# Kernel tuning notes

Hardware: AMD Instinct MI355X
Metric: run time of the kernel (lower is better)

Reference implementation:

```python
import jax, jax.numpy as jnp
import numpy as np

D_MODEL = 1024
N_HEADS = 16
D_K = D_MODEL // N_HEADS
SIGMA = 1.0
NUM_ITERS = 3
PAD_POS = 10000.0


def setup_inputs() -> dict:
    rng = jax.random.key(0)
    ks = jax.random.split(rng, 16)
    B, Lq, Lk = 8, 512, 512
    s = 1.0 / np.sqrt(D_MODEL).astype(np.float32)
    return {
        "query": jax.random.normal(ks[0], (B, Lq, D_MODEL), jnp.float32),
        "key": jax.random.normal(ks[1], (B, Lk, D_MODEL), jnp.float32),
        "value": jax.random.normal(ks[2], (B, Lk, D_MODEL), jnp.float32),
        "query_lengths": jax.random.randint(ks[3], (B,), 2, Lq),
        "key_lengths": jax.random.randint(ks[4], (B,), 2, Lk),
        "Wq": jax.random.normal(ks[5], (D_MODEL, D_MODEL), jnp.float32) * s,
        "bq": jnp.zeros((D_MODEL,), jnp.float32),
        "Wk": jax.random.normal(ks[6], (D_MODEL, D_MODEL), jnp.float32) * s,
        "bk": jnp.zeros((D_MODEL,), jnp.float32),
        "Wv": jax.random.normal(ks[7], (D_MODEL, D_MODEL), jnp.float32) * s,
        "bv": jnp.zeros((D_MODEL,), jnp.float32),
        "Wo": jax.random.normal(ks[8], (D_MODEL, D_MODEL), jnp.float32) * s,
        "bo": jnp.zeros((D_MODEL,), jnp.float32),
        "pos_scale": jnp.ones((1,), jnp.float32),
        "pos_bias": jnp.zeros((1,), jnp.float32),
    }


def _init_positions(lengths, max_len, scale, bias):
    # vectorized tcr_pep init: linspace(-L/2, L/2, L) per row, pad -> 10000
    j = jnp.arange(max_len, dtype=jnp.float32)[None, :]          # [1, L]
    L = lengths.astype(jnp.float32)[:, None]                      # [B, 1]
    step = jnp.where(L > 1.0, L / (L - 1.0), 0.0)                 # linspace step
    pos = (-L / 2.0 + j * step) * scale + bias
    pad = jnp.arange(max_len)[None, :] >= lengths[:, None]
    return jnp.where(pad, PAD_POS, pos)


def _distance_attention(qp, kp):
    d2 = (qp[:, :, None] - kp[:, None, :]) ** 2                   # [B, Lq, Lk]
    attn = jnp.exp(-d2 / (2.0 * SIGMA * SIGMA))
    masked = (qp[:, :, None] >= 1000.0) | (kp[:, None, :] >= 1000.0)
    return jnp.where(masked, 0.0, attn)


def _update_positions(qp, kp, attn):
    qn = attn / jnp.clip(attn.sum(-1, keepdims=True), 1e-9)
    qp_new = jnp.einsum('bqk,bk->bq', qn, kp)
    at = attn.transpose(0, 2, 1)
    kn = at / jnp.clip(at.sum(-1, keepdims=True), 1e-9)
    kp_new = jnp.einsum('bkq,bq->bk', kn, qp)
    qp_new = jnp.where(qp >= 1000.0, PAD_POS, qp_new)
    kp_new = jnp.where(kp >= 1000.0, PAD_POS, kp_new)
    return qp_new, kp_new


def reference(query, key, value, query_lengths, key_lengths,
              Wq, bq, Wk, bk, Wv, bv, Wo, bo, pos_scale, pos_bias):
    B, Lq, _ = query.shape
    Lk = key.shape[1]

    def split_heads(x):
        return x.reshape(B, -1, N_HEADS, D_K).transpose(0, 2, 1, 3)  # [B,H,L,Dk]

    q = split_heads(query @ Wq.T + bq)
    k = split_heads(key @ Wk.T + bk)
    v = split_heads(value @ Wv.T + bv)

    qp = _init_positions(query_lengths, Lq, pos_scale, pos_bias)  # [B, Lq]
    kp = _init_positions(key_lengths, Lk, pos_scale, pos_bias)    # [B, Lk]

    scores = jnp.einsum('bhqd,bhkd->bhqk', q, k) / jnp.sqrt(jnp.float32(D_K))
    attn = jax.nn.softmax(scores, axis=-1)                        # [B,H,Lq,Lk]

    for _ in range(NUM_ITERS):
        da = _distance_attention(qp, kp)                          # [B,Lq,Lk]
        comb = attn * da[:, None, :, :]
        comb = comb / jnp.clip(comb.sum(-1, keepdims=True), 1e-9)
        qp, kp = _update_positions(qp, kp, da)
        attn = comb

    ctx = jnp.einsum('bhqk,bhkd->bhqd', attn, v)
    ctx = ctx.transpose(0, 2, 1, 3).reshape(B, Lq, D_MODEL)
    out = ctx @ Wo.T + bo
    return out, attn.mean(axis=1)
```

## Files before the change

### kernel.cpp

```cpp
#include <hip/hip_runtime.h>
#include <math.h>

#define B_  8
#define LQ  512
#define LK  512
#define DM  1024
#define NH  16
#define DK  64
constexpr float PADP = 10000.0f;

typedef short s16x8 __attribute__((ext_vector_type(8)));
typedef float f32x4 __attribute__((ext_vector_type(4)));

__device__ inline unsigned short f2b1(float f) {
    unsigned u = __float_as_uint(f);
    unsigned r = (u + 0x7fffu + ((u >> 16) & 1u)) >> 16;
    return (unsigned short)r;
}

__global__ __launch_bounds__(256) void f2b_kernel(
    const float* __restrict__ in, unsigned short* __restrict__ out, int n4)
{
    const int i = blockIdx.x * 256 + threadIdx.x;
    if (i >= n4) return;
    const float4 v = *(const float4*)&in[(size_t)i * 4];
    ushort4 o;
    o.x = f2b1(v.x); o.y = f2b1(v.y); o.z = f2b1(v.z); o.w = f2b1(v.w);
    *(ushort4*)&out[(size_t)i * 4] = o;
}

__global__ __launch_bounds__(512) void posInit_kernel(
    const int* __restrict__ qlen, const int* __restrict__ klen,
    const float* __restrict__ pscale, const float* __restrict__ pbias,
    float* __restrict__ posQ, float* __restrict__ posK)
{
    const int b = blockIdx.x, t = threadIdx.x;
    const float scale = pscale[0], bias = pbias[0];
    {
        int ql = qlen[b];
        float Lf = (float)ql;
        float step = (Lf > 1.0f) ? Lf / (Lf - 1.0f) : 0.0f;
        float pos = (-Lf * 0.5f + (float)t * step) * scale + bias;
        posQ[b * LQ + t] = (t >= ql) ? PADP : pos;
    }
    {
        int kl = klen[b];
        float Lf = (float)kl;
        float step = (Lf > 1.0f) ? Lf / (Lf - 1.0f) : 0.0f;
        float pos = (-Lf * 0.5f + (float)t * step) * scale + bias;
        posK[b * LK + t] = (t >= kl) ? PADP : pos;
    }
}

template <bool SUMS>
__global__ __launch_bounds__(512) void daRow_kernel(
    const float* __restrict__ posQ, const float* __restrict__ posK,
    float* __restrict__ Db,
    float* __restrict__ rsB, float* __restrict__ rdB,
    float* __restrict__ colS, float* __restrict__ colD)
{
    constexpr int NCH = 16, QC = LQ / NCH;
    __shared__ float kpl[LK];
    __shared__ float csp[8][LK], cdp[8][LK];
    const int chunk = blockIdx.x, b = blockIdx.y;
    const int t = threadIdx.x, w = t >> 6, lane = t & 63;
    kpl[t] = posK[b * LK + t];
    __syncthreads();

    float cs[8] = {0,0,0,0,0,0,0,0}, cd[8] = {0,0,0,0,0,0,0,0};
    float* Dbb = Db + (size_t)b * LQ * LK;

    for (int qi = chunk * QC + w; qi < chunk * QC + QC; qi += 8) {
        const float qpv = posQ[b * LQ + qi];
        const bool qpad = (qpv >= 1000.0f);
        float rsum = 0.0f, rdot = 0.0f;
#pragma unroll
        for (int c = 0; c < 8; ++c) {
            const int k = lane + 64 * c;
            const float kpv = kpl[k];
            const float d = qpv - kpv;
            float e = (qpad || (kpv >= 1000.0f)) ? 0.0f : __expf(-0.5f * d * d);
            if (SUMS) { rsum += e; rdot += e * kpv; cs[c] += e; cd[c] += e * qpv; }
            Dbb[(size_t)qi * LK + k] = e;
        }
        if (SUMS) {
#pragma unroll
            for (int o = 32; o > 0; o >>= 1) {
                rsum += __shfl_xor(rsum, o);
                rdot += __shfl_xor(rdot, o);
            }
            if (lane == 0) { rsB[b * LQ + qi] = rsum; rdB[b * LQ + qi] = rdot; }
        }
    }
    if (SUMS) {
#pragma unroll
        for (int c = 0; c < 8; ++c) {
            csp[w][lane + 64 * c] = cs[c];
            cdp[w][lane + 64 * c] = cd[c];
        }
        __syncthreads();
        float s = 0.0f, dd = 0.0f;
        for (int ww = 0; ww < 8; ++ww) { s += csp[ww][t]; dd += cdp[ww][t]; }
        colS[((size_t)b * NCH + chunk) * LK + t] = s;
        colD[((size_t)b * NCH + chunk) * LK + t] = dd;
    }
}

__global__ __launch_bounds__(512) void posUpd_kernel(
    float* __restrict__ posQ, float* __restrict__ posK,
    const float* __restrict__ rsB, const float* __restrict__ rdB,
    const float* __restrict__ colS, const float* __restrict__ colD)
{
    constexpr int NCH = 16;
    const int b = blockIdx.x, t = threadIdx.x;
    float colsum = 0.0f, coldot = 0.0f;
#pragma unroll
    for (int c = 0; c < NCH; ++c) {
        colsum += colS[((size_t)b * NCH + c) * LK + t];
        coldot += colD[((size_t)b * NCH + c) * LK + t];
    }
    const float nk = (posK[b * LK + t] >= 1000.0f) ? PADP : coldot / fmaxf(colsum, 1e-9f);
    const float nq = (posQ[b * LQ + t] >= 1000.0f) ? PADP : rdB[b * LQ + t] / fmaxf(rsB[b * LQ + t], 1e-9f);
    posQ[b * LQ + t] = nq;
    posK[b * LK + t] = nk;
}

__global__ __launch_bounds__(256) void transpose_bf16(
    const unsigned short* __restrict__ in, unsigned short* __restrict__ out,
    int Mn, int Nn)
{
    __shared__ unsigned short tile[64][65];
    const int m0 = blockIdx.y * 64, n0 = blockIdx.x * 64;
    const int t = threadIdx.x;
    const int r = t >> 3, c8 = (t & 7) * 8;
#pragma unroll
    for (int rr = 0; rr < 64; rr += 32) {
        const uint4 v = *(const uint4*)&in[(size_t)(m0 + r + rr) * Nn + n0 + c8];
        const unsigned short* pv = (const unsigned short*)&v;
#pragma unroll
        for (int j = 0; j < 8; ++j) tile[r + rr][c8 + j] = pv[j];
    }
    __syncthreads();
#pragma unroll
    for (int rr = 0; rr < 64; rr += 32) {
        unsigned short tmp[8];
#pragma unroll
        for (int j = 0; j < 8; ++j) tmp[j] = tile[c8 + j][r + rr];
        *(uint4*)&out[(size_t)(n0 + r + rr) * Mn + m0 + c8] = *(uint4*)tmp;
    }
}

template <bool OB>
__global__ __launch_bounds__(256) void gemm_bf16_nt(
    const unsigned short* __restrict__ A,
    const unsigned short* __restrict__ Bt,
    void* __restrict__ Cv,
    const float* __restrict__ bias,
    int M, int N, int K, float alpha)
{
    constexpr int BKP = 40;
    __shared__ short As[64 * BKP];
    __shared__ short Bs[128 * BKP];
    const int m0 = blockIdx.y * 64, n0 = blockIdx.x * 128;
    const int t = threadIdx.x;
    const int wid = t >> 6, lane = t & 63;
    const int wr = wid >> 1, wc = wid & 1;
    const int lr = lane & 15, lk = (lane >> 4) * 8;

    f32x4 acc[2][4] = {};

    const int arow = t >> 2, aseg = (t & 3) * 8;
    const int brow = t >> 1, bseg = (t & 1) * 16;

    for (int kb = 0; kb < K; kb += 32) {
        const uint4 av  = *(const uint4*)&A[(size_t)(m0 + arow) * K + kb + aseg];
        const uint4 bv0 = *(const uint4*)&Bt[(size_t)(n0 + brow) * K + kb + bseg];
        const uint4 bv1 = *(const uint4*)&Bt[(size_t)(n0 + brow) * K + kb + bseg + 8];
        __syncthreads();
        *(uint4*)&As[arow * BKP + aseg] = av;
        *(uint4*)&Bs[brow * BKP + bseg] = bv0;
        *(uint4*)&Bs[brow * BKP + bseg + 8] = bv1;
        __syncthreads();

        s16x8 af[2], bf[4];
#pragma unroll
        for (int i = 0; i < 2; ++i)
            af[i] = *(const s16x8*)&As[(wr * 32 + i * 16 + lr) * BKP + lk];
#pragma unroll
        for (int j = 0; j < 4; ++j)
            bf[j] = *(const s16x8*)&Bs[(wc * 64 + j * 16 + lr) * BKP + lk];
#pragma unroll
        for (int i = 0; i < 2; ++i)
#pragma unroll
            for (int j = 0; j < 4; ++j)
                acc[i][j] = __builtin_amdgcn_mfma_f32_16x16x32_bf16(
                    af[i], bf[j], acc[i][j], 0, 0, 0);
    }

    const int r0 = (lane >> 4) * 4;
#pragma unroll
    for (int i = 0; i < 2; ++i) {
        const int row = m0 + wr * 32 + i * 16 + r0;
#pragma unroll
        for (int j = 0; j < 4; ++j) {
            const int col = n0 + wc * 64 + j * 16 + lr;
            const float bvv = bias ? bias[col] : 0.0f;
#pragma unroll
            for (int r = 0; r < 4; ++r) {
                const float val = acc[i][j][r] * alpha + bvv;
                if (OB) ((unsigned short*)Cv)[(size_t)(row + r) * N + col] = f2b1(val);
                else    ((float*)Cv)[(size_t)(row + r) * N + col] = val;
            }
        }
    }
}

__global__ __launch_bounds__(256) void scores_mfma(
    const unsigned short* __restrict__ Qb,
    const unsigned short* __restrict__ Kb,
    float* __restrict__ S, int hbase)
{
    constexpr int BKP = 72;
    __shared__ short As[128 * BKP];
    __shared__ short Bs[128 * BKP];
    const int z = blockIdx.z;
    const int b = z >> 3, hh = z & 7;
    const int hcol = (hbase + hh) * DK;
    const int m0 = blockIdx.y * 128, n0 = blockIdx.x * 128;
    const int t = threadIdx.x;
    const int wid = t >> 6, lane = t & 63;
    const int wr = wid >> 1, wc = wid & 1;
    const int lr = lane & 15, lk = (lane >> 4) * 8;

    const int srow = t >> 1, sseg = (t & 1) * 32;
    {
        const unsigned short* ag = &Qb[((size_t)(b * LQ + m0 + srow)) * DM + hcol + sseg];
        const unsigned short* bg = &Kb[((size_t)(b * LK + n0 + srow)) * DM + hcol + sseg];
#pragma unroll
        for (int s = 0; s < 4; ++s) {
            *(uint4*)&As[srow * BKP + sseg + s * 8] = *(const uint4*)(ag + s * 8);
            *(uint4*)&Bs[srow * BKP + sseg + s * 8] = *(const uint4*)(bg + s * 8);
        }
    }
    __syncthreads();

    f32x4 acc[4][4] = {};
#pragma unroll
    for (int kh = 0; kh < 2; ++kh) {
        s16x8 af[4], bf[4];
#pragma unroll
        for (int i = 0; i < 4; ++i)
            af[i] = *(const s16x8*)&As[(wr * 64 + i * 16 + lr) * BKP + kh * 32 + lk];
#pragma unroll
        for (int j = 0; j < 4; ++j)
            bf[j] = *(const s16x8*)&Bs[(wc * 64 + j * 16 + lr) * BKP + kh * 32 + lk];
#pragma unroll
        for (int i = 0; i < 4; ++i)
#pragma unroll
            for (int j = 0; j < 4; ++j)
                acc[i][j] = __builtin_amdgcn_mfma_f32_16x16x32_bf16(
                    af[i], bf[j], acc[i][j], 0, 0, 0);
    }

    const int r0 = (lane >> 4) * 4;
#pragma unroll
    for (int i = 0; i < 4; ++i) {
        const int row = m0 + wr * 64 + i * 16 + r0;
#pragma unroll
        for (int j = 0; j < 4; ++j) {
            const int col = n0 + wc * 64 + j * 16 + lr;
#pragma unroll
            for (int r = 0; r < 4; ++r)
                S[((size_t)z * LQ + row + r) * LK + col] = acc[i][j][r] * 0.125f;
        }
    }
}

__global__ __launch_bounds__(256) void ctx_mfma(
    const unsigned short* __restrict__ Ab,
    const unsigned short* __restrict__ VbT,
    unsigned short* __restrict__ ctxb, int hbase)
{
    constexpr int BKP = 72;
    __shared__ short As[64 * BKP];
    __shared__ short Bs[64 * BKP];
    const int z = blockIdx.z;
    const int b = z >> 3, hh = z & 7;
    const int hcol = (hbase + hh) * DK;
    const int q0 = blockIdx.y * 64;
    const int t = threadIdx.x;
    const int wid = t >> 6, lane = t & 63;
    const int wr = wid >> 1, wc = wid & 1;
    const int lr = lane & 15, lk = (lane >> 4) * 8;

    const unsigned short* Abase = Ab + ((size_t)z * LQ + q0) * LK;
    const unsigned short* Bbase = VbT + (size_t)hcol * (B_ * LK) + (size_t)b * LK;

    f32x4 acc[2][2] = {};
    const int srow = t >> 2, sseg = (t & 3) * 16;

    for (int kb = 0; kb < LK; kb += 64) {
        const uint4 a0 = *(const uint4*)&Abase[(size_t)srow * LK + kb + sseg];
        const uint4 a1 = *(const uint4*)&Abase[(size_t)srow * LK + kb + sseg + 8];
        const uint4 b0 = *(const uint4*)&Bbase[(size_t)srow * (B_ * LK) + kb + sseg];
        const uint4 b1 = *(const uint4*)&Bbase[(size_t)srow * (B_ * LK) + kb + sseg + 8];
        __syncthreads();
        *(uint4*)&As[srow * BKP + sseg] = a0;
        *(uint4*)&As[srow * BKP + sseg + 8] = a1;
        *(uint4*)&Bs[srow * BKP + sseg] = b0;
        *(uint4*)&Bs[srow * BKP + sseg + 8] = b1;
        __syncthreads();

#pragma unroll
        for (int kh = 0; kh < 2; ++kh) {
            s16x8 af[2], bf[2];
#pragma unroll
            for (int i = 0; i < 2; ++i)
                af[i] = *(const s16x8*)&As[(wr * 32 + i * 16 + lr) * BKP + kh * 32 + lk];
#pragma unroll
            for (int j = 0; j < 2; ++j)
                bf[j] = *(const s16x8*)&Bs[(wc * 32 + j * 16 + lr) * BKP + kh * 32 + lk];
#pragma unroll
            for (int i = 0; i < 2; ++i)
#pragma unroll
                for (int j = 0; j < 2; ++j)
                    acc[i][j] = __builtin_amdgcn_mfma_f32_16x16x32_bf16(
                        af[i], bf[j], acc[i][j], 0, 0, 0);
        }
    }

    const int r0 = (lane >> 4) * 4;
#pragma unroll
    for (int i = 0; i < 2; ++i) {
        const int row = b * LQ + q0 + wr * 32 + i * 16 + r0;
#pragma unroll
        for (int j = 0; j < 2; ++j) {
            const int col = hcol + wc * 32 + j * 16 + lr;
#pragma unroll
            for (int r = 0; r < 4; ++r)
                ctxb[(size_t)(row + r) * DM + col] = f2b1(acc[i][j][r]);
        }
    }
}

template <bool BT>
__global__ __launch_bounds__(256) void gemm64(
    const float* __restrict__ A, int lda, long aS1, long aS2,
    const float* __restrict__ Bm, int ldb, long bS1, long bS2,
    float* __restrict__ C, int ldc, long cS1, long cS2,
    const float* __restrict__ bias, int K, float alpha, int zshift)
{
    const int z = blockIdx.z;
    const long z1 = z >> zshift;
    const long z2 = z & ((1 << zshift) - 1);
    A  += z1 * aS1 + z2 * aS2;
    Bm += z1 * bS1 + z2 * bS2;
    C  += z1 * cS1 + z2 * cS2;

    const int m0 = blockIdx.y * 64, n0 = blockIdx.x * 64;
    __shared__ float As[32][68];
    __shared__ float Bs[32][68];
    const int t = threadIdx.x;
    const int ty = t >> 4, tx = t & 15;

    float acc[4][4];
#pragma unroll
    for (int i = 0; i < 4; ++i)
#pragma unroll
        for (int j = 0; j < 4; ++j) acc[i][j] = 0.0f;

    const int mA = t >> 3;
    const int kA = (t & 7) * 4;

    for (int kb = 0; kb < K; kb += 32) {
        {
            const float4 a0 = *(const float4*)&A[(size_t)(m0 + mA) * lda + kb + kA];
            const float4 a1 = *(const float4*)&A[(size_t)(m0 + mA + 32) * lda + kb + kA];
            As[kA + 0][mA] = a0.x; As[kA + 1][mA] = a0.y; As[kA + 2][mA] = a0.z; As[kA + 3][mA] = a0.w;
            As[kA + 0][mA + 32] = a1.x; As[kA + 1][mA + 32] = a1.y; As[kA + 2][mA + 32] = a1.z; As[kA + 3][mA + 32] = a1.w;
        }
        if (BT) {
            const float4 b0 = *(const float4*)&Bm[(size_t)(n0 + mA) * ldb + kb + kA];
            const float4 b1 = *(const float4*)&Bm[(size_t)(n0 + mA + 32) * ldb + kb + kA];
            Bs[kA + 0][mA] = b0.x; Bs[kA + 1][mA] = b0.y; Bs[kA + 2][mA] = b0.z; Bs[kA + 3][mA] = b0.w;
            Bs[kA + 0][mA + 32] = b1.x; Bs[kA + 1][mA + 32] = b1.y; Bs[kA + 2][mA + 32] = b1.z; Bs[kA + 3][mA + 32] = b1.w;
        } else {
            const int kB = t >> 4;
            const int nB = (t & 15) * 4;
            const float4 b0 = *(const float4*)&Bm[(size_t)(kb + kB) * ldb + n0 + nB];
            const float4 b1 = *(const float4*)&Bm[(size_t)(kb + kB + 16) * ldb + n0 + nB];
            *(float4*)&Bs[kB][nB] = b0;
            *(float4*)&Bs[kB + 16][nB] = b1;
        }
        __syncthreads();

#pragma unroll
        for (int kk = 0; kk < 32; ++kk) {
            const float4 av = *(const float4*)&As[kk][ty * 4];
            const float4 bv = *(const float4*)&Bs[kk][tx * 4];
            const float a[4] = {av.x, av.y, av.z, av.w};
            const float bb[4] = {bv.x, bv.y, bv.z, bv.w};
#pragma unroll
            for (int i = 0; i < 4; ++i)
#pragma unroll
                for (int j = 0; j < 4; ++j)
                    acc[i][j] = fmaf(a[i], bb[j], acc[i][j]);
        }
        __syncthreads();
    }

#pragma unroll
    for (int i = 0; i < 4; ++i) {
        const int row = m0 + ty * 4 + i;
        float4 o;
        o.x = acc[i][0] * alpha;
        o.y = acc[i][1] * alpha;
        o.z = acc[i][2] * alpha;
        o.w = acc[i][3] * alpha;
        if (bias) {
            o.x += bias[n0 + tx * 4 + 0];
            o.y += bias[n0 + tx * 4 + 1];
            o.z += bias[n0 + tx * 4 + 2];
            o.w += bias[n0 + tx * 4 + 3];
        }
        *(float4*)&C[(size_t)row * ldc + n0 + tx * 4] = o;
    }
}

template <bool BF16OUT>
__global__ __launch_bounds__(256) void softmaxP_kernel(
    float* __restrict__ S, const float* __restrict__ D,
    void* __restrict__ AOut, float* __restrict__ meanOut,
    int nheads, int accumulate)
{
    const int b = blockIdx.x >> 9, q = blockIdx.x & 511;
    const int t = threadIdx.x, w = t >> 6, lane = t & 63;
    __shared__ float Pl[3][LK];
    __shared__ float part[4][LK];
    const size_t NPB = (size_t)B_ * LQ * LK;
    const size_t rowoff = ((size_t)b * LQ + q) * LK;

    for (int i = t; i < LK; i += 256) {
        Pl[0][i] = D[rowoff + i];
        Pl[1][i] = D[NPB + rowoff + i];
        Pl[2][i] = D[2 * NPB + rowoff + i];
    }
    __syncthreads();

    float macc[8];
#pragma unroll
    for (int j = 0; j < 8; ++j) macc[j] = 0.0f;

    for (int h = w; h < nheads; h += 4) {
        const size_t roff = (((size_t)b * nheads + h) * LQ + q) * LK;
        const float* row = S + roff;
        float v[8];
        const float4 s0 = *(const float4*)&row[lane * 8];
        const float4 s1 = *(const float4*)&row[lane * 8 + 4];
        v[0] = s0.x; v[1] = s0.y; v[2] = s0.z; v[3] = s0.w;
        v[4] = s1.x; v[5] = s1.y; v[6] = s1.z; v[7] = s1.w;
        float mx = v[0];
#pragma unroll
        for (int j = 1; j < 8; ++j) mx = fmaxf(mx, v[j]);
#pragma unroll
        for (int o = 32; o > 0; o >>= 1) mx = fmaxf(mx, __shfl_xor(mx, o));
        float zz = 0.0f;
#pragma unroll
        for (int j = 0; j < 8; ++j) { v[j] = __expf(v[j] - mx); zz += v[j]; }
#pragma unroll
        for (int o = 32; o > 0; o >>= 1) zz += __shfl_xor(zz, o);
        const float invz = 1.0f / zz;
#pragma unroll
        for (int j = 0; j < 8; ++j) v[j] *= invz;

#pragma unroll
        for (int it = 0; it < 3; ++it) {
            float s = 0.0f;
#pragma unroll
            for (int j = 0; j < 8; ++j) {
                v[j] *= Pl[it][lane * 8 + j];
                s += v[j];
            }
#pragma unroll
            for (int o = 32; o > 0; o >>= 1) s += __shfl_xor(s, o);
            const float inv = 1.0f / fmaxf(s, 1e-9f);
#pragma unroll
            for (int j = 0; j < 8; ++j) v[j] *= inv;
        }

#pragma unroll
        for (int j = 0; j < 8; ++j) macc[j] += v[j];

        if (BF16OUT) {
            unsigned short* arow = (unsigned short*)AOut + roff;
            ushort4 u0, u1;
            u0.x = f2b1(v[0]); u0.y = f2b1(v[1]); u0.z = f2b1(v[2]); u0.w = f2b1(v[3]);
            u1.x = f2b1(v[4]); u1.y = f2b1(v[5]); u1.z = f2b1(v[6]); u1.w = f2b1(v[7]);
            *(ushort4*)&arow[lane * 8] = u0;
            *(ushort4*)&arow[lane * 8 + 4] = u1;
        } else {
            float* arow = (float*)AOut + roff;
            *(float4*)&arow[lane * 8] = make_float4(v[0], v[1], v[2], v[3]);
            *(float4*)&arow[lane * 8 + 4] = make_float4(v[4], v[5], v[6], v[7]);
        }
    }

    *(float4*)&part[w][lane * 8] = make_float4(macc[0], macc[1], macc[2], macc[3]);
    *(float4*)&part[w][lane * 8 + 4] = make_float4(macc[4], macc[5], macc[6], macc[7]);
    __syncthreads();

    for (int i = t; i < LK; i += 256) {
        const float m = (part[0][i] + part[1][i] + part[2][i] + part[3][i]) * (1.0f / 16.0f);
        const size_t oi = ((size_t)b * LQ + q) * LK + i;
        meanOut[oi] = accumulate ? (meanOut[oi] + m) : m;
    }
}

extern "C" void kernel_launch(void* const* d_in, const int* in_sizes, int n_in,
                              void* d_out, int out_size, void* d_ws, size_t ws_size,
                              hipStream_t stream)
{
    const float* query  = (const float*)d_in[0];
    const float* key    = (const float*)d_in[1];
    const float* value  = (const float*)d_in[2];
    const int*   qlen   = (const int*)d_in[3];
    const int*   klen   = (const int*)d_in[4];
    const float* Wq     = (const float*)d_in[5];
    const float* bq     = (const float*)d_in[6];
    const float* Wk     = (const float*)d_in[7];
    const float* bk     = (const float*)d_in[8];
    const float* Wv     = (const float*)d_in[9];
    const float* bv     = (const float*)d_in[10];
    const float* Wo     = (const float*)d_in[11];
    const float* bo     = (const float*)d_in[12];
    const float* pscale = (const float*)d_in[13];
    const float* pbias  = (const float*)d_in[14];

    float* out     = (float*)d_out;
    float* meanOut = out + (size_t)B_ * LQ * DM;

    const size_t NQKV = (size_t)B_ * LQ * DM;
    const size_t NP   = (size_t)B_ * LQ * LK;
    const size_t NW   = (size_t)DM * DM;
    const size_t NSg  = (size_t)B_ * 8 * LQ * LK;

    float* Dbuf = (float*)d_ws;
    float* posQ = Dbuf + 3 * NP;
    float* posK = posQ + B_ * LQ;
    float* rsB  = posK + B_ * LK;
    float* rdB  = rsB + B_ * LQ;
    float* colS = rdB + B_ * LQ;
    float* colD = colS + (size_t)B_ * 16 * LK;
    float* fend = colD + (size_t)B_ * 16 * LK;
    unsigned short* Qb   = (unsigned short*)fend;
    unsigned short* Kb   = Qb + NQKV;
    unsigned short* Vb   = Kb + NQKV;
    unsigned short* VbT  = Vb + NQKV;
    unsigned short* ctxb = VbT + NQKV;
    unsigned short* wqb  = ctxb + NQKV;
    unsigned short* wkb  = wqb + NW;
    unsigned short* wvb  = wkb + NW;
    unsigned short* wob  = wvb + NW;
    unsigned short* Ab   = wob + NW;
    float* Sg = (float*)(Ab + NSg);
    unsigned short* xq = Ab;
    unsigned short* xk = xq + NQKV;
    unsigned short* xv = xk + NQKV;

    const size_t need_full = (size_t)((char*)(Sg + NSg) - (char*)d_ws);

    if (ws_size >= need_full) {
        posInit_kernel<<<B_, 512, 0, stream>>>(qlen, klen, pscale, pbias, posQ, posK);
        dim3 gDa(16, B_);
        daRow_kernel<true><<<gDa, 512, 0, stream>>>(posQ, posK, Dbuf, rsB, rdB, colS, colD);
        posUpd_kernel<<<B_, 512, 0, stream>>>(posQ, posK, rsB, rdB, colS, colD);
        daRow_kernel<true><<<gDa, 512, 0, stream>>>(posQ, posK, Dbuf + NP, rsB, rdB, colS, colD);
        posUpd_kernel<<<B_, 512, 0, stream>>>(posQ, posK, rsB, rdB, colS, colD);
        daRow_kernel<false><<<gDa, 512, 0, stream>>>(posQ, posK, Dbuf + 2 * NP, rsB, rdB, colS, colD);

        const int gX = (int)(NQKV / 4 / 256);
        const int gW = (int)(NW / 4 / 256);
        f2b_kernel<<<gX, 256, 0, stream>>>(query, xq, (int)(NQKV / 4));
        f2b_kernel<<<gX, 256, 0, stream>>>(key,   xk, (int)(NQKV / 4));
        f2b_kernel<<<gX, 256, 0, stream>>>(value, xv, (int)(NQKV / 4));
        f2b_kernel<<<gW, 256, 0, stream>>>(Wq, wqb, (int)(NW / 4));
        f2b_kernel<<<gW, 256, 0, stream>>>(Wk, wkb, (int)(NW / 4));
        f2b_kernel<<<gW, 256, 0, stream>>>(Wv, wvb, (int)(NW / 4));
        f2b_kernel<<<gW, 256, 0, stream>>>(Wo, wob, (int)(NW / 4));

        dim3 gP(DM / 128, (B_ * LQ) / 64);
        gemm_bf16_nt<true><<<gP, 256, 0, stream>>>(xq, wqb, Qb, bq, B_ * LQ, DM, DM, 1.0f);
        gemm_bf16_nt<true><<<gP, 256, 0, stream>>>(xk, wkb, Kb, bk, B_ * LQ, DM, DM, 1.0f);
        gemm_bf16_nt<true><<<gP, 256, 0, stream>>>(xv, wvb, Vb, bv, B_ * LQ, DM, DM, 1.0f);

        dim3 gT(DM / 64, (B_ * LK) / 64);
        transpose_bf16<<<gT, 256, 0, stream>>>(Vb, VbT, B_ * LK, DM);

        for (int g = 0; g < 2; ++g) {
            dim3 gS(LK / 128, LQ / 128, B_ * 8);
            scores_mfma<<<gS, 256, 0, stream>>>(Qb, Kb, Sg, g * 8);
            softmaxP_kernel<true><<<B_ * LQ, 256, 0, stream>>>(Sg, Dbuf, Ab, meanOut, 8, g);
            dim3 gC(1, LQ / 64, B_ * 8);
            ctx_mfma<<<gC, 256, 0, stream>>>(Ab, VbT, ctxb, g * 8);
        }

        gemm_bf16_nt<false><<<gP, 256, 0, stream>>>(ctxb, wob, out, bo, B_ * LQ, DM, DM, 1.0f);
        return;
    }

    float* qbuf = (float*)d_ws;
    float* kbuf = qbuf + NQKV;
    float* vbuf = kbuf + NQKV;
    float* Dfb  = vbuf + NQKV;
    float* Sfb  = Dfb + 3 * NP;
    float* ctxbuf = Sfb + NP;
    float* pQ = ctxbuf + NQKV;
    float* pK = pQ + B_ * LQ;
    float* rS = pK + B_ * LK;
    float* rD = rS + B_ * LQ;
    float* cS = rD + B_ * LQ;
    float* cD = cS + (size_t)B_ * 16 * LK;

    posInit_kernel<<<B_, 512, 0, stream>>>(qlen, klen, pscale, pbias, pQ, pK);
    dim3 gDa(16, B_);
    daRow_kernel<true><<<gDa, 512, 0, stream>>>(pQ, pK, Dfb, rS, rD, cS, cD);
    posUpd_kernel<<<B_, 512, 0, stream>>>(pQ, pK, rS, rD, cS, cD);
    daRow_kernel<true><<<gDa, 512, 0, stream>>>(pQ, pK, Dfb + NP, rS, rD, cS, cD);
    posUpd_kernel<<<B_, 512, 0, stream>>>(pQ, pK, rS, rD, cS, cD);
    daRow_kernel<false><<<gDa, 512, 0, stream>>>(pQ, pK, Dfb + 2 * NP, rS, rD, cS, cD);

    dim3 gProj(DM / 64, (B_ * LQ) / 64, 1);
    gemm64<true><<<gProj, 256, 0, stream>>>(query, DM, 0, 0, Wq, DM, 0, 0,
                                            qbuf, DM, 0, 0, bq, DM, 1.0f, 0);
    gemm64<true><<<gProj, 256, 0, stream>>>(key, DM, 0, 0, Wk, DM, 0, 0,
                                            kbuf, DM, 0, 0, bk, DM, 1.0f, 0);
    gemm64<true><<<gProj, 256, 0, stream>>>(value, DM, 0, 0, Wv, DM, 0, 0,
                                            vbuf, DM, 0, 0, bv, DM, 1.0f, 0);
    for (int h = 0; h < NH; ++h) {
        dim3 gS2(LK / 64, LQ / 64, B_);
        gemm64<true><<<gS2, 256, 0, stream>>>(
            qbuf + h * DK, DM, (long)LQ * DM, 0,
            kbuf + h * DK, DM, (long)LK * DM, 0,
            Sfb, LK, (long)LQ * LK, 0,
            nullptr, DK, 0.125f, 0);
        softmaxP_kernel<false><<<B_ * LQ, 256, 0, stream>>>(Sfb, Dfb, Sfb, meanOut, 1, h > 0 ? 1 : 0);
        dim3 gC2(1, LQ / 64, B_);
        gemm64<false><<<gC2, 256, 0, stream>>>(
            Sfb, LK, (long)LQ * LK, 0,
            vbuf + h * DK, DM, (long)LK * DM, 0,
            ctxbuf + h * DK, DM, (long)LQ * DM, 0,
            nullptr, LK, 1.0f, 0);
    }
    dim3 gO(DM / 64, (B_ * LQ) / 64, 1);
    gemm64<true><<<gO, 256, 0, stream>>>(ctxbuf, DM, 0, 0, Wo, DM, 0, 0,
                                         out, DM, 0, 0, bo, DM, 1.0f, 0);
}
```

Before: 257.0 us.

## Fuse position init/update into distance kernels and batch conversions and QKV GEMMs

New measurement: 325.3 us. +26.6%, slower.

```diff
diff --git a/kernel.cpp b/kernel.cpp
--- a/kernel.cpp
+++ b/kernel.cpp
@@ -18,60 +18,94 @@
     return (unsigned short)r;
 }
 
-__global__ __launch_bounds__(256) void f2b_kernel(
-    const float* __restrict__ in, unsigned short* __restrict__ out, int n4)
-{
+__global__ __launch_bounds__(256) void f2b_all_kernel(
+    const float* __restrict__ query, const float* __restrict__ key,
+    const float* __restrict__ value,
+    const float* __restrict__ Wq, const float* __restrict__ Wk,
+    const float* __restrict__ Wv, const float* __restrict__ Wo,
+    unsigned short* __restrict__ xq, unsigned short* __restrict__ xk,
+    unsigned short* __restrict__ xv,
+    unsigned short* __restrict__ wqb, unsigned short* __restrict__ wkb,
+    unsigned short* __restrict__ wvb, unsigned short* __restrict__ wob)
+{
+    const int s = blockIdx.y;
+    const float* src;
+    unsigned short* dst;
+    if (s < 4)       { src = query + ((size_t)s << 20);       dst = xq + ((size_t)s << 20); }
+    else if (s < 8)  { src = key   + ((size_t)(s - 4) << 20); dst = xk + ((size_t)(s - 4) << 20); }
+    else if (s < 12) { src = value + ((size_t)(s - 8) << 20); dst = xv + ((size_t)(s - 8) << 20); }
+    else {
+        const int w = s - 12;
+        src = (w == 0) ? Wq : (w == 1) ? Wk : (w == 2) ? Wv : Wo;
+        dst = (w == 0) ? wqb : (w == 1) ? wkb : (w == 2) ? wvb : wob;
+    }
     const int i = blockIdx.x * 256 + threadIdx.x;
-    if (i >= n4) return;
-    const float4 v = *(const float4*)&in[(size_t)i * 4];
+    const float4 v = *(const float4*)&src[(size_t)i * 4];
     ushort4 o;
     o.x = f2b1(v.x); o.y = f2b1(v.y); o.z = f2b1(v.z); o.w = f2b1(v.w);
-    *(ushort4*)&out[(size_t)i * 4] = o;
-}
-
-__global__ __launch_bounds__(512) void posInit_kernel(
+    *(ushort4*)&dst[(size_t)i * 4] = o;
+}
+
+template <int PHASE>
+__global__ __launch_bounds__(512) void daRow_kernel(
     const int* __restrict__ qlen, const int* __restrict__ klen,
     const float* __restrict__ pscale, const float* __restrict__ pbias,
-    float* __restrict__ posQ, float* __restrict__ posK)
-{
-    const int b = blockIdx.x, t = threadIdx.x;
-    const float scale = pscale[0], bias = pbias[0];
-    {
-        int ql = qlen[b];
-        float Lf = (float)ql;
-        float step = (Lf > 1.0f) ? Lf / (Lf - 1.0f) : 0.0f;
-        float pos = (-Lf * 0.5f + (float)t * step) * scale + bias;
-        posQ[b * LQ + t] = (t >= ql) ? PADP : pos;
-    }
-    {
-        int kl = klen[b];
-        float Lf = (float)kl;
-        float step = (Lf > 1.0f) ? Lf / (Lf - 1.0f) : 0.0f;
-        float pos = (-Lf * 0.5f + (float)t * step) * scale + bias;
-        posK[b * LK + t] = (t >= kl) ? PADP : pos;
-    }
-}
-
-template <bool SUMS>
-__global__ __launch_bounds__(512) void daRow_kernel(
-    const float* __restrict__ posQ, const float* __restrict__ posK,
-    float* __restrict__ Db,
-    float* __restrict__ rsB, float* __restrict__ rdB,
-    float* __restrict__ colS, float* __restrict__ colD)
+    float* __restrict__ posQ,
+    const float* __restrict__ posKin, float* __restrict__ posKout,
+    const float* __restrict__ rsIn, const float* __restrict__ rdIn,
+    const float* __restrict__ colSIn, const float* __restrict__ colDIn,
+    float* __restrict__ rsOut, float* __restrict__ rdOut,
+    float* __restrict__ colSOut, float* __restrict__ colDOut,
+    float* __restrict__ Dplane)
 {
     constexpr int NCH = 16, QC = LQ / NCH;
     __shared__ float kpl[LK];
     __shared__ float csp[8][LK], cdp[8][LK];
     const int chunk = blockIdx.x, b = blockIdx.y;
     const int t = threadIdx.x, w = t >> 6, lane = t & 63;
-    kpl[t] = posK[b * LK + t];
+
+    float scale = 0.0f, bias = 0.0f;
+    if (PHASE == 0) { scale = pscale[0]; bias = pbias[0]; }
+
+    if (PHASE == 0) {
+        const int kl = klen[b];
+        const float Lf = (float)kl;
+        const float step = (Lf > 1.0f) ? Lf / (Lf - 1.0f) : 0.0f;
+        const float pos = (-Lf * 0.5f + (float)t * step) * scale + bias;
+        const float kv = (t >= kl) ? PADP : pos;
+        kpl[t] = kv;
+        if (chunk == 0) posKout[b * LK + t] = kv;
+    } else {
+        float colsum = 0.0f, coldot = 0.0f;
+#pragma unroll
+        for (int c = 0; c < NCH; ++c) {
+            colsum += colSIn[((size_t)b * NCH + c) * LK + t];
+            coldot += colDIn[((size_t)b * NCH + c) * LK + t];
+        }
+        const float prev = posKin[b * LK + t];
+        const float kv = (prev >= 1000.0f) ? PADP : coldot / fmaxf(colsum, 1e-9f);
+        kpl[t] = kv;
+        if (PHASE == 1 && chunk == 0) posKout[b * LK + t] = kv;
+    }
     __syncthreads();
 
     float cs[8] = {0,0,0,0,0,0,0,0}, cd[8] = {0,0,0,0,0,0,0,0};
-    float* Dbb = Db + (size_t)b * LQ * LK;
+    float* Dbb = Dplane + (size_t)b * LQ * LK;
 
     for (int qi = chunk * QC + w; qi < chunk * QC + QC; qi += 8) {
-        const float qpv = posQ[b * LQ + qi];
+        float qpv;
+        if (PHASE == 0) {
+            const int ql = qlen[b];
+            const float Lf = (float)ql;
+            const float step = (Lf > 1.0f) ? Lf / (Lf - 1.0f) : 0.0f;
+            qpv = (qi >= ql) ? PADP : (-Lf * 0.5f + (float)qi * step) * scale + bias;
+            if (lane == 0) posQ[b * LQ + qi] = qpv;
+        } else {
+            const float prev = posQ[b * LQ + qi];
+            qpv = (prev >= 1000.0f) ? PADP
+                : rdIn[b * LQ + qi] / fmaxf(rsIn[b * LQ + qi], 1e-9f);
+            if (PHASE == 1 && lane == 0) posQ[b * LQ + qi] = qpv;
+        }
         const bool qpad = (qpv >= 1000.0f);
         float rsum = 0.0f, rdot = 0.0f;
 #pragma unroll
@@ -80,19 +114,19 @@
             const float kpv = kpl[k];
             const float d = qpv - kpv;
             float e = (qpad || (kpv >= 1000.0f)) ? 0.0f : __expf(-0.5f * d * d);
-            if (SUMS) { rsum += e; rdot += e * kpv; cs[c] += e; cd[c] += e * qpv; }
+            if (PHASE < 2) { rsum += e; rdot += e * kpv; cs[c] += e; cd[c] += e * qpv; }
             Dbb[(size_t)qi * LK + k] = e;
         }
-        if (SUMS) {
+        if (PHASE < 2) {
 #pragma unroll
             for (int o = 32; o > 0; o >>= 1) {
                 rsum += __shfl_xor(rsum, o);
                 rdot += __shfl_xor(rdot, o);
             }
-            if (lane == 0) { rsB[b * LQ + qi] = rsum; rdB[b * LQ + qi] = rdot; }
-        }
-    }
-    if (SUMS) {
+            if (lane == 0) { rsOut[b * LQ + qi] = rsum; rdOut[b * LQ + qi] = rdot; }
+        }
+    }
+    if (PHASE < 2) {
 #pragma unroll
         for (int c = 0; c < 8; ++c) {
             csp[w][lane + 64 * c] = cs[c];
@@ -101,28 +135,9 @@
         __syncthreads();
         float s = 0.0f, dd = 0.0f;
         for (int ww = 0; ww < 8; ++ww) { s += csp[ww][t]; dd += cdp[ww][t]; }
-        colS[((size_t)b * NCH + chunk) * LK + t] = s;
-        colD[((size_t)b * NCH + chunk) * LK + t] = dd;
-    }
-}
-
-__global__ __launch_bounds__(512) void posUpd_kernel(
-    float* __restrict__ posQ, float* __restrict__ posK,
-    const float* __restrict__ rsB, const float* __restrict__ rdB,
-    const float* __restrict__ colS, const float* __restrict__ colD)
-{
-    constexpr int NCH = 16;
-    const int b = blockIdx.x, t = threadIdx.x;
-    float colsum = 0.0f, coldot = 0.0f;
-#pragma unroll
-    for (int c = 0; c < NCH; ++c) {
-        colsum += colS[((size_t)b * NCH + c) * LK + t];
-        coldot += colD[((size_t)b * NCH + c) * LK + t];
-    }
-    const float nk = (posK[b * LK + t] >= 1000.0f) ? PADP : coldot / fmaxf(colsum, 1e-9f);
-    const float nq = (posQ[b * LQ + t] >= 1000.0f) ? PADP : rdB[b * LQ + t] / fmaxf(rsB[b * LQ + t], 1e-9f);
-    posQ[b * LQ + t] = nq;
-    posK[b * LK + t] = nk;
+        colSOut[((size_t)b * NCH + chunk) * LK + t] = s;
+        colDOut[((size_t)b * NCH + chunk) * LK + t] = dd;
+    }
 }
 
 __global__ __launch_bounds__(256) void transpose_bf16(
@@ -150,49 +165,63 @@
     }
 }
 
-template <bool OB>
+template <int BN, bool OB>
 __global__ __launch_bounds__(256) void gemm_bf16_nt(
-    const unsigned short* __restrict__ A,
-    const unsigned short* __restrict__ Bt,
-    void* __restrict__ Cv,
-    const float* __restrict__ bias,
-    int M, int N, int K, float alpha)
+    const unsigned short* __restrict__ A0, const unsigned short* __restrict__ B0,
+    void* __restrict__ C0, const float* __restrict__ bias0,
+    const unsigned short* __restrict__ A1, const unsigned short* __restrict__ B1,
+    void* __restrict__ C1, const float* __restrict__ bias1,
+    const unsigned short* __restrict__ A2, const unsigned short* __restrict__ B2,
+    void* __restrict__ C2, const float* __restrict__ bias2,
+    int M, int N, int K)
 {
     constexpr int BKP = 40;
+    constexpr int JT = BN / 32;
+    constexpr int TPR = 256 / BN;
     __shared__ short As[64 * BKP];
-    __shared__ short Bs[128 * BKP];
-    const int m0 = blockIdx.y * 64, n0 = blockIdx.x * 128;
+    __shared__ short Bs[BN * BKP];
+
+    const unsigned short* A; const unsigned short* Bt; void* Cv; const float* bias;
+    if (blockIdx.z == 0)      { A = A0; Bt = B0; Cv = C0; bias = bias0; }
+    else if (blockIdx.z == 1) { A = A1; Bt = B1; Cv = C1; bias = bias1; }
+    else                      { A = A2; Bt = B2; Cv = C2; bias = bias2; }
+
+    const int m0 = blockIdx.y * 64, n0 = blockIdx.x * BN;
     const int t = threadIdx.x;
     const int wid = t >> 6, lane = t & 63;
     const int wr = wid >> 1, wc = wid & 1;
     const int lr = lane & 15, lk = (lane >> 4) * 8;
 
-    f32x4 acc[2][4] = {};
+    f32x4 acc[2][JT] = {};
 
     const int arow = t >> 2, aseg = (t & 3) * 8;
-    const int brow = t >> 1, bseg = (t & 1) * 16;
+    const int brow = t / TPR;
+    const int bc0 = (t % TPR) * (32 / TPR);
 
     for (int kb = 0; kb < K; kb += 32) {
-        const uint4 av  = *(const uint4*)&A[(size_t)(m0 + arow) * K + kb + aseg];
-        const uint4 bv0 = *(const uint4*)&Bt[(size_t)(n0 + brow) * K + kb + bseg];
-        const uint4 bv1 = *(const uint4*)&Bt[(size_t)(n0 + brow) * K + kb + bseg + 8];
+        const uint4 av = *(const uint4*)&A[(size_t)(m0 + arow) * K + kb + aseg];
+        uint4 bv[32 / TPR / 8];
+#pragma unroll
+        for (int u = 0; u < 32 / TPR / 8; ++u)
+            bv[u] = *(const uint4*)&Bt[(size_t)(n0 + brow) * K + kb + bc0 + u * 8];
         __syncthreads();
         *(uint4*)&As[arow * BKP + aseg] = av;
-        *(uint4*)&Bs[brow * BKP + bseg] = bv0;
-        *(uint4*)&Bs[brow * BKP + bseg + 8] = bv1;
+#pragma unroll
+        for (int u = 0; u < 32 / TPR / 8; ++u)
+            *(uint4*)&Bs[brow * BKP + bc0 + u * 8] = bv[u];
         __syncthreads();
 
-        s16x8 af[2], bf[4];
+        s16x8 af[2], bf[JT];
 #pragma unroll
         for (int i = 0; i < 2; ++i)
             af[i] = *(const s16x8*)&As[(wr * 32 + i * 16 + lr) * BKP + lk];
 #pragma unroll
-        for (int j = 0; j < 4; ++j)
-            bf[j] = *(const s16x8*)&Bs[(wc * 64 + j * 16 + lr) * BKP + lk];
+        for (int j = 0; j < JT; ++j)
+            bf[j] = *(const s16x8*)&Bs[(wc * (BN / 2) + j * 16 + lr) * BKP + lk];
 #pragma unroll
         for (int i = 0; i < 2; ++i)
 #pragma unroll
-            for (int j = 0; j < 4; ++j)
+            for (int j = 0; j < JT; ++j)
                 acc[i][j] = __builtin_amdgcn_mfma_f32_16x16x32_bf16(
                     af[i], bf[j], acc[i][j], 0, 0, 0);
     }
@@ -202,12 +231,12 @@
     for (int i = 0; i < 2; ++i) {
         const int row = m0 + wr * 32 + i * 16 + r0;
 #pragma unroll
-        for (int j = 0; j < 4; ++j) {
-            const int col = n0 + wc * 64 + j * 16 + lr;
+        for (int j = 0; j < JT; ++j) {
+            const int col = n0 + wc * (BN / 2) + j * 16 + lr;
             const float bvv = bias ? bias[col] : 0.0f;
 #pragma unroll
             for (int r = 0; r < 4; ++r) {
-                const float val = acc[i][j][r] * alpha + bvv;
+                const float val = acc[i][j][r] + bvv;
                 if (OB) ((unsigned short*)Cv)[(size_t)(row + r) * N + col] = f2b1(val);
                 else    ((float*)Cv)[(size_t)(row + r) * N + col] = val;
             }
@@ -543,15 +572,22 @@
     const size_t NP   = (size_t)B_ * LQ * LK;
     const size_t NW   = (size_t)DM * DM;
     const size_t NSg  = (size_t)B_ * 8 * LQ * LK;
-
-    float* Dbuf = (float*)d_ws;
-    float* posQ = Dbuf + 3 * NP;
-    float* posK = posQ + B_ * LQ;
-    float* rsB  = posK + B_ * LK;
-    float* rdB  = rsB + B_ * LQ;
-    float* colS = rdB + B_ * LQ;
-    float* colD = colS + (size_t)B_ * 16 * LK;
-    float* fend = colD + (size_t)B_ * 16 * LK;
+    const size_t NPOS = (size_t)B_ * LQ;
+    const size_t NCOL = (size_t)B_ * 16 * LK;
+
+    float* Dbuf  = (float*)d_ws;
+    float* posQ  = Dbuf + 3 * NP;
+    float* posK1 = posQ + NPOS;
+    float* posK2 = posK1 + NPOS;
+    float* rs1   = posK2 + NPOS;
+    float* rd1   = rs1 + NPOS;
+    float* rs2   = rd1 + NPOS;
+    float* rd2   = rs2 + NPOS;
+    float* colS1 = rd2 + NPOS;
+    float* colD1 = colS1 + NCOL;
+    float* colS2 = colD1 + NCOL;
+    float* colD2 = colS2 + NCOL;
+    float* fend  = colD2 + NCOL;
     unsigned short* Qb   = (unsigned short*)fend;
     unsigned short* Kb   = Qb + NQKV;
     unsigned short* Vb   = Kb + NQKV;
@@ -570,28 +606,28 @@
     const size_t need_full = (size_t)((char*)(Sg + NSg) - (char*)d_ws);
 
     if (ws_size >= need_full) {
-        posInit_kernel<<<B_, 512, 0, stream>>>(qlen, klen, pscale, pbias, posQ, posK);
         dim3 gDa(16, B_);
-        daRow_kernel<true><<<gDa, 512, 0, stream>>>(posQ, posK, Dbuf, rsB, rdB, colS, colD);
-        posUpd_kernel<<<B_, 512, 0, stream>>>(posQ, posK, rsB, rdB, colS, colD);
-        daRow_kernel<true><<<gDa, 512, 0, stream>>>(posQ, posK, Dbuf + NP, rsB, rdB, colS, colD);
-        posUpd_kernel<<<B_, 512, 0, stream>>>(posQ, posK, rsB, rdB, colS, colD);
-        daRow_kernel<false><<<gDa, 512, 0, stream>>>(posQ, posK, Dbuf + 2 * NP, rsB, rdB, colS, colD);
-
-        const int gX = (int)(NQKV / 4 / 256);
-        const int gW = (int)(NW / 4 / 256);
-        f2b_kernel<<<gX, 256, 0, stream>>>(query, xq, (int)(NQKV / 4));
-        f2b_kernel<<<gX, 256, 0, stream>>>(key,   xk, (int)(NQKV / 4));
-        f2b_kernel<<<gX, 256, 0, stream>>>(value, xv, (int)(NQKV / 4));
-        f2b_kernel<<<gW, 256, 0, stream>>>(Wq, wqb, (int)(NW / 4));
-        f2b_kernel<<<gW, 256, 0, stream>>>(Wk, wkb, (int)(NW / 4));
-        f2b_kernel<<<gW, 256, 0, stream>>>(Wv, wvb, (int)(NW / 4));
-        f2b_kernel<<<gW, 256, 0, stream>>>(Wo, wob, (int)(NW / 4));
-
-        dim3 gP(DM / 128, (B_ * LQ) / 64);
-        gemm_bf16_nt<true><<<gP, 256, 0, stream>>>(xq, wqb, Qb, bq, B_ * LQ, DM, DM, 1.0f);
-        gemm_bf16_nt<true><<<gP, 256, 0, stream>>>(xk, wkb, Kb, bk, B_ * LQ, DM, DM, 1.0f);
-        gemm_bf16_nt<true><<<gP, 256, 0, stream>>>(xv, wvb, Vb, bv, B_ * LQ, DM, DM, 1.0f);
+        daRow_kernel<0><<<gDa, 512, 0, stream>>>(qlen, klen, pscale, pbias,
+            posQ, nullptr, posK1,
+            nullptr, nullptr, nullptr, nullptr,
+            rs1, rd1, colS1, colD1, Dbuf);
+        daRow_kernel<1><<<gDa, 512, 0, stream>>>(qlen, klen, pscale, pbias,
+            posQ, posK1, posK2,
+            rs1, rd1, colS1, colD1,
+            rs2, rd2, colS2, colD2, Dbuf + NP);
+        daRow_kernel<2><<<gDa, 512, 0, stream>>>(qlen, klen, pscale, pbias,
+            posQ, posK2, nullptr,
+            rs2, rd2, colS2, colD2,
+            nullptr, nullptr, nullptr, nullptr, Dbuf + 2 * NP);
+
+        dim3 gF(1024, 16);
+        f2b_all_kernel<<<gF, 256, 0, stream>>>(query, key, value, Wq, Wk, Wv, Wo,
+                                               xq, xk, xv, wqb, wkb, wvb, wob);
+
+        dim3 gP(DM / 256, (B_ * LQ) / 64, 3);
+        gemm_bf16_nt<256, true><<<gP, 256, 0, stream>>>(
+            xq, wqb, Qb, bq, xk, wkb, Kb, bk, xv, wvb, Vb, bv,
+            B_ * LQ, DM, DM);
 
         dim3 gT(DM / 64, (B_ * LK) / 64);
         transpose_bf16<<<gT, 256, 0, stream>>>(Vb, VbT, B_ * LK, DM);
@@ -604,7 +640,10 @@
             ctx_mfma<<<gC, 256, 0, stream>>>(Ab, VbT, ctxb, g * 8);
         }
 
-        gemm_bf16_nt<false><<<gP, 256, 0, stream>>>(ctxb, wob, out, bo, B_ * LQ, DM, DM, 1.0f);
+        dim3 gO(DM / 128, (B_ * LQ) / 64, 1);
+        gemm_bf16_nt<128, false><<<gO, 256, 0, stream>>>(
+            ctxb, wob, out, bo, ctxb, wob, out, bo, ctxb, wob, out, bo,
+            B_ * LQ, DM, DM);
         return;
     }
 
@@ -614,20 +653,28 @@
     float* Dfb  = vbuf + NQKV;
     float* Sfb  = Dfb + 3 * NP;
     float* ctxbuf = Sfb + NP;
-    float* pQ = ctxbuf + NQKV;
-    float* pK = pQ + B_ * LQ;
-    float* rS = pK + B_ * LK;
-    float* rD = rS + B_ * LQ;
-    float* cS = rD + B_ * LQ;
-    float* cD = cS + (size_t)B_ * 16 * LK;
-
-    posInit_kernel<<<B_, 512, 0, stream>>>(qlen, klen, pscale, pbias, pQ, pK);
+    float* pQ  = ctxbuf + NQKV;
+    float* pK1 = pQ + NPOS;
+    float* pK2 = pK1 + NPOS;
+    float* frs1 = pK2 + NPOS;
+    float* frd1 = frs1 + NPOS;
+    float* frs2 = frd1 + NPOS;
+    float* frd2 = frs2 + NPOS;
+    float* fcS1 = frd2 + NPOS;
+    float* fcD1 = fcS1 + NCOL;
+    float* fcS2 = fcD1 + NCOL;
+    float* fcD2 = fcS2 + NCOL;
+
     dim3 gDa(16, B_);
-    daRow_kernel<true><<<gDa, 512, 0, stream>>>(pQ, pK, Dfb, rS, rD, cS, cD);
-    posUpd_kernel<<<B_, 512, 0, stream>>>(pQ, pK, rS, rD, cS, cD);
-    daRow_kernel<true><<<gDa, 512, 0, stream>>>(pQ, pK, Dfb + NP, rS, rD, cS, cD);
-    posUpd_kernel<<<B_, 512, 0, stream>>>(pQ, pK, rS, rD, cS, cD);
-    daRow_kernel<false><<<gDa, 512, 0, stream>>>(pQ, pK, Dfb + 2 * NP, rS, rD, cS, cD);
+    daRow_kernel<0><<<gDa, 512, 0, stream>>>(qlen, klen, pscale, pbias,
+        pQ, nullptr, pK1, nullptr, nullptr, nullptr, nullptr,
+        frs1, frd1, fcS1, fcD1, Dfb);
+    daRow_kernel<1><<<gDa, 512, 0, stream>>>(qlen, klen, pscale, pbias,
+        pQ, pK1, pK2, frs1, frd1, fcS1, fcD1,
+        frs2, frd2, fcS2, fcD2, Dfb + NP);
+    daRow_kernel<2><<<gDa, 512, 0, stream>>>(qlen, klen, pscale, pbias,
+        pQ, pK2, nullptr, frs2, frd2, fcS2, fcD2,
+        nullptr, nullptr, nullptr, nullptr, Dfb + 2 * NP);
 
     dim3 gProj(DM / 64, (B_ * LQ) / 64, 1);
     gemm64<true><<<gProj, 256, 0, stream>>>(query, DM, 0, 0, Wq, DM, 0, 0,
```
